# Kernel optimization log

Measured on AMD Instinct MI355X. Metric: run time of the kernel, lower is better.

The kernel has to match this reference:

```python
import jax, jax.numpy as jnp
import numpy as np

N_NODES = 50000
N_EDGES = 800000
D_IN = 128
D_HID = 128
D_OUT = 128
N_GRAPHS = 512


def _linear_params(key, d_in, d_out):
    kw, kb = jax.random.split(key)
    bound = 1.0 / np.sqrt(d_in)
    W = jax.random.uniform(kw, (d_in, d_out), minval=-bound, maxval=bound, dtype=jnp.float32)
    b = jax.random.uniform(kb, (d_out,), minval=-bound, maxval=bound, dtype=jnp.float32)
    return W, b


def setup_inputs() -> dict:
    key = jax.random.key(0)
    ks = jax.random.split(key, 8)
    x = jax.random.normal(ks[0], (N_NODES, D_IN), dtype=jnp.float32)
    edge_index = jax.random.randint(ks[1], (2, N_EDGES), 0, N_NODES, dtype=jnp.int64)
    batch = jnp.sort(jax.random.randint(ks[2], (N_NODES,), 0, N_GRAPHS, dtype=jnp.int64))
    W1a, b1a = _linear_params(ks[3], D_IN, D_HID)
    W1b, b1b = _linear_params(ks[4], D_HID, D_HID)
    W2a, b2a = _linear_params(ks[5], D_HID, D_HID)
    W2b, b2b = _linear_params(ks[6], D_HID, D_OUT)
    Wfc, bfc = _linear_params(ks[7], D_OUT, D_OUT)
    return {"x": x, "edge_index": edge_index, "batch": batch,
            "W1a": W1a, "b1a": b1a, "W1b": W1b, "b1b": b1b,
            "W2a": W2a, "b2a": b2a, "W2b": W2b, "b2b": b2b,
            "Wfc": Wfc, "bfc": bfc}


def _gin_conv(h, src, dst, Wa, ba, Wb, bb):
    # neighbor sum: gather source features, scatter-add to targets (eps=0)
    agg = jax.ops.segment_sum(h[src], dst, num_segments=N_NODES)
    z = h + agg  # (1+eps)*x + sum_neighbors, eps=0
    z = jax.nn.relu(z @ Wa + ba)
    return z @ Wb + bb


def reference(x, edge_index, batch, W1a, b1a, W1b, b1b, W2a, b2a, W2b, b2b, Wfc, bfc):
    src, dst = edge_index[0], edge_index[1]
    h = jax.nn.relu(_gin_conv(x, src, dst, W1a, b1a, W1b, b1b))
    h = jax.nn.relu(_gin_conv(h, src, dst, W2a, b2a, W2b, b2b))
    g = jax.ops.segment_sum(h, batch, num_segments=N_GRAPHS)  # global_add_pool
    return jax.nn.relu(g @ Wfc + bfc)
```

## Files before the change

kernel.cpp:

```cpp
#include <hip/hip_runtime.h>

#define N_NODES 50000
#define N_EDGES 800000
#define N_GRAPHS 512
#define CAP 48

typedef __bf16 bf16x8 __attribute__((ext_vector_type(8)));
typedef float f32x4 __attribute__((ext_vector_type(4)));
typedef unsigned short u16;
typedef unsigned int u32;

__device__ __forceinline__ u16 f2bf(float f) {
    union { float f; u32 i; } v; v.f = f;
    u32 r = v.i + 0x7fffu + ((v.i >> 16) & 1u);
    return (u16)(r >> 16);
}
__device__ __forceinline__ float bf2f(u16 u) {
    union { u32 i; float f; } v; v.i = ((u32)u) << 16; return v.f;
}

__global__ void k_prep(const int* __restrict__ ei, int* __restrict__ cnt, u16* __restrict__ slots,
                       const float* __restrict__ X, u16* __restrict__ XB,
                       const float* __restrict__ W1a, const float* __restrict__ W1b,
                       const float* __restrict__ W2a, const float* __restrict__ W2b,
                       u16* __restrict__ T1a, u16* __restrict__ T1b,
                       u16* __restrict__ T2a, u16* __restrict__ T2b,
                       int E, int n4) {
    int bid = blockIdx.x;
    if (bid < 3125) {
        int e = bid * 256 + threadIdx.x;
        if (e < E) {
            int s = ei[e];
            int d = ei[E + e];
            int p = atomicAdd(&cnt[d * 4], 1);
            if (p < CAP) slots[(size_t)d * CAP + p] = (u16)s;
        }
    } else if (bid < 9375) {
        int i = (bid - 3125) * 256 + threadIdx.x;
        if (i < n4) {
            float4 v = ((const float4*)X)[i];
            ushort4 o;
            o.x = f2bf(v.x); o.y = f2bf(v.y); o.z = f2bf(v.z); o.w = f2bf(v.w);
            ((ushort4*)XB)[i] = o;
        }
    } else {
        int b2 = bid - 9375;
        int widx = b2 >> 6;
        int i = (b2 & 63) * 256 + threadIdx.x;
        const float* W = widx == 0 ? W1a : widx == 1 ? W1b : widx == 2 ? W2a : W2b;
        u16* T = widx == 0 ? T1a : widx == 1 ? T1b : widx == 2 ? T2a : T2b;
        int k = i >> 7, n = i & 127;
        T[n * 128 + k] = f2bf(W[k * 128 + n]);
    }
}

__global__ void k_agg(const u16* __restrict__ X, const int* __restrict__ cnt,
                      const u16* __restrict__ slots, u16* __restrict__ Z, int N) {
    int wid = (blockIdx.x * blockDim.x + threadIdx.x) >> 6;
    if (wid >= N) return;
    int lane = threadIdx.x & 63;
    const u32* X2 = (const u32*)X;
    u32 v = X2[(size_t)wid * 64 + lane];
    float ax = bf2f((u16)(v & 0xffff));
    float ay = bf2f((u16)(v >> 16));
    int deg = cnt[wid * 4];
    if (deg > CAP) deg = CAP;
    int idx = (lane < deg) ? (int)slots[(size_t)wid * CAP + lane] : 0;
    int j = 0;
    for (; j + 16 <= deg; j += 16) {
        u32 t[16];
#pragma unroll
        for (int u = 0; u < 16; ++u)
            t[u] = X2[(size_t)__shfl(idx, j + u) * 64 + lane];
        float sx = 0.f, sy = 0.f;
#pragma unroll
        for (int u = 0; u < 16; ++u) {
            sx += bf2f((u16)(t[u] & 0xffff));
            sy += bf2f((u16)(t[u] >> 16));
        }
        ax += sx; ay += sy;
    }
    for (; j + 4 <= deg; j += 4) {
        u32 t0 = X2[(size_t)__shfl(idx, j    ) * 64 + lane];
        u32 t1 = X2[(size_t)__shfl(idx, j + 1) * 64 + lane];
        u32 t2 = X2[(size_t)__shfl(idx, j + 2) * 64 + lane];
        u32 t3 = X2[(size_t)__shfl(idx, j + 3) * 64 + lane];
        ax += bf2f((u16)(t0 & 0xffff)) + bf2f((u16)(t1 & 0xffff))
            + bf2f((u16)(t2 & 0xffff)) + bf2f((u16)(t3 & 0xffff));
        ay += bf2f((u16)(t0 >> 16)) + bf2f((u16)(t1 >> 16))
            + bf2f((u16)(t2 >> 16)) + bf2f((u16)(t3 >> 16));
    }
    for (; j < deg; ++j) {
        u32 u = X2[(size_t)__shfl(idx, j) * 64 + lane];
        ax += bf2f((u16)(u & 0xffff));
        ay += bf2f((u16)(u >> 16));
    }
    ((u32*)Z)[(size_t)wid * 64 + lane] = (((u32)f2bf(ay)) << 16) | (u32)f2bf(ax);
}

__global__ __launch_bounds__(256, 1)
void k_mlp(const u16* __restrict__ Z, const u16* __restrict__ WaT,
           const float* __restrict__ ba, const u16* __restrict__ WbT,
           const float* __restrict__ bb, u16* __restrict__ H, int N) {
    __shared__ u16 smZ[128 * 128];
    __shared__ u16 smW[128 * 128];
    uint4* smZ4 = (uint4*)smZ;
    uint4* smW4 = (uint4*)smW;

    const int tid = threadIdx.x;
    const int lane = tid & 63, wv = tid >> 6;
    const int q = lane >> 4, m = lane & 15;
    const int row0 = blockIdx.x * 128;

    for (int i = tid; i < 2048; i += 256) {
        int r = i >> 4, c4 = i & 15;
        smW4[r * 16 + (c4 ^ (r & 15))] = ((const uint4*)WaT)[i];
    }
    for (int i = tid; i < 2048; i += 256) {
        int r = i >> 4, c4 = i & 15;
        int gr = row0 + r;
        uint4 v = make_uint4(0u, 0u, 0u, 0u);
        if (gr < N) v = ((const uint4*)Z)[(size_t)gr * 16 + c4];
        smZ4[r * 16 + (c4 ^ (r & 15))] = v;
    }
    __syncthreads();

    f32x4 acc[2][8];
    for (int rt = 0; rt < 2; ++rt)
        for (int nt = 0; nt < 8; ++nt)
            acc[rt][nt] = (f32x4){0.f, 0.f, 0.f, 0.f};
    for (int kt = 0; kt < 4; ++kt) {
        bf16x8 a[2];
        for (int rt = 0; rt < 2; ++rt) {
            int r = wv * 32 + rt * 16 + m;
            a[rt] = *(const bf16x8*)(smZ4 + (r * 16 + ((kt * 4 + q) ^ (r & 15))));
        }
        for (int nt = 0; nt < 8; ++nt) {
            int n = nt * 16 + m;
            bf16x8 bfr = *(const bf16x8*)(smW4 + (n * 16 + ((kt * 4 + q) ^ (n & 15))));
            for (int rt = 0; rt < 2; ++rt)
                acc[rt][nt] = __builtin_amdgcn_mfma_f32_16x16x32_bf16(a[rt], bfr, acc[rt][nt], 0, 0, 0);
        }
    }
    __syncthreads();

    for (int i = tid; i < 2048; i += 256) {
        int r = i >> 4, c4 = i & 15;
        smW4[r * 16 + (c4 ^ (r & 15))] = ((const uint4*)WbT)[i];
    }
    for (int nt = 0; nt < 8; ++nt) {
        int col = nt * 16 + m;
        float bias = ba[col];
        int c4 = col >> 3, ci = col & 7;
        for (int rt = 0; rt < 2; ++rt)
            for (int r2 = 0; r2 < 4; ++r2) {
                int row = wv * 32 + rt * 16 + q * 4 + r2;
                float x = acc[rt][nt][r2] + bias;
                x = x > 0.f ? x : 0.f;
                smZ[(row * 16 + (c4 ^ (row & 15))) * 8 + ci] = f2bf(x);
            }
    }
    __syncthreads();

    f32x4 acc2[2][8];
    for (int rt = 0; rt < 2; ++rt)
        for (int nt = 0; nt < 8; ++nt)
            acc2[rt][nt] = (f32x4){0.f, 0.f, 0.f, 0.f};
    for (int kt = 0; kt < 4; ++kt) {
        bf16x8 a[2];
        for (int rt = 0; rt < 2; ++rt) {
            int r = wv * 32 + rt * 16 + m;
            a[rt] = *(const bf16x8*)(smZ4 + (r * 16 + ((kt * 4 + q) ^ (r & 15))));
        }
        for (int nt = 0; nt < 8; ++nt) {
            int n = nt * 16 + m;
            bf16x8 bfr = *(const bf16x8*)(smW4 + (n * 16 + ((kt * 4 + q) ^ (n & 15))));
            for (int rt = 0; rt < 2; ++rt)
                acc2[rt][nt] = __builtin_amdgcn_mfma_f32_16x16x32_bf16(a[rt], bfr, acc2[rt][nt], 0, 0, 0);
        }
    }
    for (int nt = 0; nt < 8; ++nt) {
        int col = nt * 16 + m;
        float bias = bb[col];
        for (int rt = 0; rt < 2; ++rt)
            for (int r2 = 0; r2 < 4; ++r2) {
                int row = row0 + wv * 32 + rt * 16 + q * 4 + r2;
                if (row < N) {
                    float x = acc2[rt][nt][r2] + bias;
                    H[(size_t)row * 128 + col] = f2bf(x > 0.f ? x : 0.f);
                }
            }
    }
}

__global__ __launch_bounds__(256, 1)
void k_mlp2(const u16* __restrict__ Z, const u16* __restrict__ WaT,
            const float* __restrict__ ba, const u16* __restrict__ WbT,
            const float* __restrict__ bb, const int* __restrict__ batch,
            float* __restrict__ G, int N) {
    __shared__ u16 smZ[128 * 128];
    __shared__ u16 smW[128 * 128];
    __shared__ int sb[128];
    uint4* smZ4 = (uint4*)smZ;
    uint4* smW4 = (uint4*)smW;

    const int tid = threadIdx.x;
    const int lane = tid & 63, wv = tid >> 6;
    const int q = lane >> 4, m = lane & 15;
    const int row0 = blockIdx.x * 128;

    if (tid < 128) sb[tid] = (row0 + tid < N) ? batch[row0 + tid] : -1;

    for (int i = tid; i < 2048; i += 256) {
        int r = i >> 4, c4 = i & 15;
        smW4[r * 16 + (c4 ^ (r & 15))] = ((const uint4*)WaT)[i];
    }
    for (int i = tid; i < 2048; i += 256) {
        int r = i >> 4, c4 = i & 15;
        int gr = row0 + r;
        uint4 v = make_uint4(0u, 0u, 0u, 0u);
        if (gr < N) v = ((const uint4*)Z)[(size_t)gr * 16 + c4];
        smZ4[r * 16 + (c4 ^ (r & 15))] = v;
    }
    __syncthreads();

    f32x4 acc[2][8];
    for (int rt = 0; rt < 2; ++rt)
        for (int nt = 0; nt < 8; ++nt)
            acc[rt][nt] = (f32x4){0.f, 0.f, 0.f, 0.f};
    for (int kt = 0; kt < 4; ++kt) {
        bf16x8 a[2];
        for (int rt = 0; rt < 2; ++rt) {
            int r = wv * 32 + rt * 16 + m;
            a[rt] = *(const bf16x8*)(smZ4 + (r * 16 + ((kt * 4 + q) ^ (r & 15))));
        }
        for (int nt = 0; nt < 8; ++nt) {
            int n = nt * 16 + m;
            bf16x8 bfr = *(const bf16x8*)(smW4 + (n * 16 + ((kt * 4 + q) ^ (n & 15))));
            for (int rt = 0; rt < 2; ++rt)
                acc[rt][nt] = __builtin_amdgcn_mfma_f32_16x16x32_bf16(a[rt], bfr, acc[rt][nt], 0, 0, 0);
        }
    }
    __syncthreads();

    for (int i = tid; i < 2048; i += 256) {
        int r = i >> 4, c4 = i & 15;
        smW4[r * 16 + (c4 ^ (r & 15))] = ((const uint4*)WbT)[i];
    }
    for (int nt = 0; nt < 8; ++nt) {
        int col = nt * 16 + m;
        float bias = ba[col];
        int c4 = col >> 3, ci = col & 7;
        for (int rt = 0; rt < 2; ++rt)
            for (int r2 = 0; r2 < 4; ++r2) {
                int row = wv * 32 + rt * 16 + q * 4 + r2;
                float x = acc[rt][nt][r2] + bias;
                x = x > 0.f ? x : 0.f;
                smZ[(row * 16 + (c4 ^ (row & 15))) * 8 + ci] = f2bf(x);
            }
    }
    __syncthreads();

    f32x4 acc2[2][8];
    for (int rt = 0; rt < 2; ++rt)
        for (int nt = 0; nt < 8; ++nt)
            acc2[rt][nt] = (f32x4){0.f, 0.f, 0.f, 0.f};
    for (int kt = 0; kt < 4; ++kt) {
        bf16x8 a[2];
        for (int rt = 0; rt < 2; ++rt) {
            int r = wv * 32 + rt * 16 + m;
            a[rt] = *(const bf16x8*)(smZ4 + (r * 16 + ((kt * 4 + q) ^ (r & 15))));
        }
        for (int nt = 0; nt < 8; ++nt) {
            int n = nt * 16 + m;
            bf16x8 bfr = *(const bf16x8*)(smW4 + (n * 16 + ((kt * 4 + q) ^ (n & 15))));
            for (int rt = 0; rt < 2; ++rt)
                acc2[rt][nt] = __builtin_amdgcn_mfma_f32_16x16x32_bf16(a[rt], bfr, acc2[rt][nt], 0, 0, 0);
        }
    }
    for (int nt = 0; nt < 8; ++nt) {
        int col = nt * 16 + m;
        float bias = bb[col];
        for (int rt = 0; rt < 2; ++rt)
#pragma unroll
            for (int r2 = 0; r2 < 4; ++r2) {
                int row = wv * 32 + rt * 16 + q * 4 + r2;
                float x = acc2[rt][nt][r2] + bias;
                smZ[row * 128 + col] = f2bf(x > 0.f ? x : 0.f);
            }
    }
    __syncthreads();
    {
        int col = tid & 127, half = tid >> 7;
        int rbeg = half * 64, rend = rbeg + 64;
        float run = 0.f; int curg = -1;
        for (int r = rbeg; r < rend; ++r) {
            int gg = sb[r];
            if (gg < 0) break;
            if (gg != curg) {
                if (curg >= 0) atomicAdd(&G[curg * 128 + col], run);
                run = 0.f; curg = gg;
            }
            run += bf2f(smZ[r * 128 + col]);
        }
        if (curg >= 0) atomicAdd(&G[curg * 128 + col], run);
    }
}

__global__ void k_fc(const float* __restrict__ G, const float* __restrict__ W,
                     const float* __restrict__ bias, float* __restrict__ O) {
    __shared__ float gs[128];
    int t = threadIdx.x, gidx = blockIdx.x;
    gs[t] = G[gidx * 128 + t];
    __syncthreads();
    float acc = bias[t];
    for (int k = 0; k < 128; ++k)
        acc += gs[k] * W[k * 128 + t];
    acc = acc > 0.f ? acc : 0.f;
    O[gidx * 128 + t] = acc;
}

extern "C" void kernel_launch(void* const* d_in, const int* in_sizes, int n_in,
                              void* d_out, int out_size, void* d_ws, size_t ws_size,
                              hipStream_t stream) {
    const int N = N_NODES, E = N_EDGES, NG = N_GRAPHS;

    const float* x   = (const float*)d_in[0];
    const int* ei    = (const int*)d_in[1];
    const int* batch = (const int*)d_in[2];
    const float* W1a = (const float*)d_in[3];
    const float* b1a = (const float*)d_in[4];
    const float* W1b = (const float*)d_in[5];
    const float* b1b = (const float*)d_in[6];
    const float* W2a = (const float*)d_in[7];
    const float* b2a = (const float*)d_in[8];
    const float* W2b = (const float*)d_in[9];
    const float* b2b = (const float*)d_in[10];
    const float* Wfc = (const float*)d_in[11];
    const float* bfc = (const float*)d_in[12];
    float* out = (float*)d_out;

    char* w = (char*)d_ws;
    int* cnt    = (int*)(w + 0x0000000);
    float* g    = (float*)(w + 0x00C4000);
    u16* slots  = (u16*)(w + 0x0110000);
    u16* xb     = (u16*)(w + 0x05B0000);
    u16* zb     = (u16*)(w + 0x1280000);
    u16* hb     = (u16*)(w + 0x1F50000);
    u16* T1a    = (u16*)(w + 0x2C20000);
    u16* T1b    = (u16*)(w + 0x2C28000);
    u16* T2a    = (u16*)(w + 0x2C30000);
    u16* T2b    = (u16*)(w + 0x2C38000);

    hipMemsetAsync(w, 0, 0x104000, stream);

    const int n4 = N * 128 / 4;
    k_prep<<<9631, 256, 0, stream>>>(ei, cnt, slots, x, xb, W1a, W1b, W2a, W2b,
                                     T1a, T1b, T2a, T2b, E, n4);

    const int AGGB = (N * 64 + 255) / 256;
    const int MLPB = (N + 127) / 128;

    k_agg<<<AGGB, 256, 0, stream>>>(xb, cnt, slots, zb, N);
    k_mlp<<<MLPB, 256, 0, stream>>>(zb, T1a, b1a, T1b, b1b, hb, N);
    k_agg<<<AGGB, 256, 0, stream>>>(hb, cnt, slots, xb, N);
    k_mlp2<<<MLPB, 256, 0, stream>>>(xb, T2a, b2a, T2b, b2b, batch, g, N);

    k_fc<<<NG, 128, 0, stream>>>(g, Wfc, bfc, out);
}
```

Measured before the change: 236.4 us.

## Bin edge-slot atomics per XCC and compact into per-node neighbor lists

Edge bucketing now spreads atomic counters and slot writes across eight per-XCC bins, chosen by reading the hardware XCC id register. This keeps atomics local to each die's L2 instead of contending across dies. A new compaction kernel merges the per-bin slots plus an overflow buffer into a dense per-node list and degree array for the aggregation kernels. The change also sets launch bounds to two blocks per CU on the MLP kernels. It adds an extra kernel launch, a larger memset and more workspace, and falls back to the old path if the workspace is too small.

```diff
diff --git a/kernel.cpp b/kernel.cpp
--- a/kernel.cpp
+++ b/kernel.cpp
@@ -3,7 +3,8 @@
 #define N_NODES 50000
 #define N_EDGES 800000
 #define N_GRAPHS 512
-#define CAP 48
+#define CAP8 24
+#define CAPF 48
 
 typedef __bf16 bf16x8 __attribute__((ext_vector_type(8)));
 typedef float f32x4 __attribute__((ext_vector_type(4)));
@@ -19,21 +20,35 @@
     union { u32 i; float f; } v; v.i = ((u32)u) << 16; return v.f;
 }
 
-__global__ void k_prep(const int* __restrict__ ei, int* __restrict__ cnt, u16* __restrict__ slots,
+__global__ void k_prep(const int* __restrict__ ei, int* __restrict__ cnt,
+                       u16* __restrict__ slots8, u16* __restrict__ ovf,
                        const float* __restrict__ X, u16* __restrict__ XB,
                        const float* __restrict__ W1a, const float* __restrict__ W1b,
                        const float* __restrict__ W2a, const float* __restrict__ W2b,
                        u16* __restrict__ T1a, u16* __restrict__ T1b,
                        u16* __restrict__ T2a, u16* __restrict__ T2b,
-                       int E, int n4) {
+                       int E, int n4, int big) {
     int bid = blockIdx.x;
     if (bid < 3125) {
         int e = bid * 256 + threadIdx.x;
         if (e < E) {
             int s = ei[e];
             int d = ei[E + e];
-            int p = atomicAdd(&cnt[d * 4], 1);
-            if (p < CAP) slots[(size_t)d * CAP + p] = (u16)s;
+            if (big) {
+                u32 xcc;
+                asm volatile("s_getreg_b32 %0, hwreg(20, 0, 32)" : "=s"(xcc));
+                int bin = (int)(xcc & 7u);
+                int p = atomicAdd(&cnt[bin * N_NODES + d], 1);
+                if (p < CAP8) {
+                    slots8[((size_t)bin * N_NODES + d) * CAP8 + p] = (u16)s;
+                } else {
+                    int p2 = atomicAdd(&cnt[8 * N_NODES + d], 1);
+                    if (p2 < CAPF) ovf[(size_t)d * CAPF + p2] = (u16)s;
+                }
+            } else {
+                int p = atomicAdd(&cnt[d * 4], 1);
+                if (p < CAPF) slots8[(size_t)d * CAPF + p] = (u16)s;
+            }
         }
     } else if (bid < 9375) {
         int i = (bid - 3125) * 256 + threadIdx.x;
@@ -54,7 +69,32 @@
     }
 }
 
-__global__ void k_agg(const u16* __restrict__ X, const int* __restrict__ cnt,
+__global__ void k_compact(const int* __restrict__ cnt, const u16* __restrict__ slots8,
+                          const u16* __restrict__ ovf, int* __restrict__ deg,
+                          u16* __restrict__ comp) {
+    int node = (blockIdx.x * 256 + threadIdx.x) >> 6;
+    int lane = threadIdx.x & 63;
+    if (node >= N_NODES) return;
+    int cval = (lane < 9) ? cnt[lane * N_NODES + node] : 0;
+    int total = 0, seg = -1, off = 0;
+#pragma unroll
+    for (int sgi = 0; sgi < 9; ++sgi) {
+        int cs = __shfl(cval, sgi);
+        int cap = (sgi == 8) ? CAPF : CAP8;
+        cs = cs < cap ? cs : cap;
+        if (lane >= total && lane < total + cs) { seg = sgi; off = lane - total; }
+        total += cs;
+    }
+    if (total > CAPF) total = CAPF;
+    if (lane == 0) deg[node] = total;
+    if (seg >= 0 && lane < CAPF) {
+        u16 v = (seg == 8) ? ovf[(size_t)node * CAPF + off]
+                           : slots8[((size_t)seg * N_NODES + node) * CAP8 + off];
+        comp[(size_t)node * CAPF + lane] = v;
+    }
+}
+
+__global__ void k_agg(const u16* __restrict__ X, const int* __restrict__ deg_arr, int dstride,
                       const u16* __restrict__ slots, u16* __restrict__ Z, int N) {
     int wid = (blockIdx.x * blockDim.x + threadIdx.x) >> 6;
     if (wid >= N) return;
@@ -63,9 +103,9 @@
     u32 v = X2[(size_t)wid * 64 + lane];
     float ax = bf2f((u16)(v & 0xffff));
     float ay = bf2f((u16)(v >> 16));
-    int deg = cnt[wid * 4];
-    if (deg > CAP) deg = CAP;
-    int idx = (lane < deg) ? (int)slots[(size_t)wid * CAP + lane] : 0;
+    int deg = deg_arr[wid * dstride];
+    if (deg > CAPF) deg = CAPF;
+    int idx = (lane < deg) ? (int)slots[(size_t)wid * CAPF + lane] : 0;
     int j = 0;
     for (; j + 16 <= deg; j += 16) {
         u32 t[16];
@@ -98,7 +138,7 @@
     ((u32*)Z)[(size_t)wid * 64 + lane] = (((u32)f2bf(ay)) << 16) | (u32)f2bf(ax);
 }
 
-__global__ __launch_bounds__(256, 1)
+__global__ __launch_bounds__(256, 2)
 void k_mlp(const u16* __restrict__ Z, const u16* __restrict__ WaT,
            const float* __restrict__ ba, const u16* __restrict__ WbT,
            const float* __restrict__ bb, u16* __restrict__ H, int N) {
@@ -193,7 +233,7 @@
     }
 }
 
-__global__ __launch_bounds__(256, 1)
+__global__ __launch_bounds__(256, 2)
 void k_mlp2(const u16* __restrict__ Z, const u16* __restrict__ WaT,
             const float* __restrict__ ba, const u16* __restrict__ WbT,
             const float* __restrict__ bb, const int* __restrict__ batch,
@@ -341,29 +381,56 @@
     float* out = (float*)d_out;
 
     char* w = (char*)d_ws;
-    int* cnt    = (int*)(w + 0x0000000);
-    float* g    = (float*)(w + 0x00C4000);
-    u16* slots  = (u16*)(w + 0x0110000);
-    u16* xb     = (u16*)(w + 0x05B0000);
-    u16* zb     = (u16*)(w + 0x1280000);
-    u16* hb     = (u16*)(w + 0x1F50000);
-    u16* T1a    = (u16*)(w + 0x2C20000);
-    u16* T1b    = (u16*)(w + 0x2C28000);
-    u16* T2a    = (u16*)(w + 0x2C30000);
-    u16* T2b    = (u16*)(w + 0x2C38000);
-
-    hipMemsetAsync(w, 0, 0x104000, stream);
+    auto al = [](size_t v) { return (v + 255) & ~(size_t)255; };
+
+    int* cnt   = (int*)(w + 0);
+    float* g   = (float*)(w + 0x1C0000);
+    size_t off = 0x200000;
+
+    size_t slots8B = (size_t)8 * N * CAP8 * 2;
+    size_t ovfB    = (size_t)N * CAPF * 2;
+    size_t compB   = (size_t)N * CAPF * 2;
+    size_t degB    = (size_t)N * 4;
+    size_t featB   = (size_t)N * 128 * 2;
+    size_t bigNeed = al(off) + al(slots8B) + al(ovfB) + al(compB) + al(degB)
+                   + 3 * al(featB) + 4 * al(32768);
+    const int big = (ws_size >= bigNeed) ? 1 : 0;
+
+    u16* slots8 = (u16*)(w + off);
+    off += big ? al(slots8B) : al((size_t)N * CAPF * 2);
+    u16* ovf  = (u16*)(w + off); if (big) off += al(ovfB);
+    u16* comp = (u16*)(w + off); if (big) off += al(compB);
+    int* deg  = (int*)(w + off); if (big) off += al(degB);
+    u16* xb   = (u16*)(w + off); off += al(featB);
+    u16* zb   = (u16*)(w + off); off += al(featB);
+    u16* hb   = (u16*)(w + off); off += al(featB);
+    u16* T1a  = (u16*)(w + off); off += al(32768);
+    u16* T1b  = (u16*)(w + off); off += al(32768);
+    u16* T2a  = (u16*)(w + off); off += al(32768);
+    u16* T2b  = (u16*)(w + off); off += al(32768);
+
+    hipMemsetAsync(w, 0, 0x200000, stream);
 
     const int n4 = N * 128 / 4;
-    k_prep<<<9631, 256, 0, stream>>>(ei, cnt, slots, x, xb, W1a, W1b, W2a, W2b,
-                                     T1a, T1b, T2a, T2b, E, n4);
+    k_prep<<<9631, 256, 0, stream>>>(ei, cnt, slots8, ovf, x, xb, W1a, W1b, W2a, W2b,
+                                     T1a, T1b, T2a, T2b, E, n4, big);
+
+    const u16* aggSlots;
+    const int* aggDeg;
+    int dstride;
+    if (big) {
+        k_compact<<<(N * 64 + 255) / 256, 256, 0, stream>>>(cnt, slots8, ovf, deg, comp);
+        aggSlots = comp; aggDeg = deg; dstride = 1;
+    } else {
+        aggSlots = slots8; aggDeg = cnt; dstride = 4;
+    }
 
     const int AGGB = (N * 64 + 255) / 256;
     const int MLPB = (N + 127) / 128;
 
-    k_agg<<<AGGB, 256, 0, stream>>>(xb, cnt, slots, zb, N);
+    k_agg<<<AGGB, 256, 0, stream>>>(xb, aggDeg, dstride, aggSlots, zb, N);
     k_mlp<<<MLPB, 256, 0, stream>>>(zb, T1a, b1a, T1b, b1b, hb, N);
-    k_agg<<<AGGB, 256, 0, stream>>>(hb, cnt, slots, xb, N);
+    k_agg<<<AGGB, 256, 0, stream>>>(hb, aggDeg, dstride, aggSlots, xb, N);
     k_mlp2<<<MLPB, 256, 0, stream>>>(xb, T2a, b2a, T2b, b2b, batch, g, N);
 
     k_fc<<<NG, 128, 0, stream>>>(g, Wfc, bfc, out);
```

After: 253.5 us. 1.07x slower.
